# Kernel optimization log

Measured on AMD Instinct MI355X. Metric: run time of the kernel, lower is better.

Reference implementation:

```python
import jax, jax.numpy as jnp
import numpy as np
import math

B_, L_, CSEQ, CMETH = 1, 16384, 5, 3
DM, NL, DI, N, R, K = 256, 6, 512, 16, 32, 4


def setup_inputs():
    key = jax.random.key(0)
    ks = jax.random.split(key, 16)
    s = lambda k, shape, sc=0.02: jax.random.normal(k, shape, jnp.float32) * sc
    # torch-style dt bias init: softplus(bias) in [0.001, 0.1]
    dt_init = jnp.exp(jax.random.uniform(ks[0], (NL, DI)) * (math.log(0.1) - math.log(0.001)) + math.log(0.001))
    dtproj_b = dt_init + jnp.log(-jnp.expm1(-dt_init))
    A = jnp.broadcast_to(jnp.arange(1, N + 1, dtype=jnp.float32), (NL, DI, N))
    return {
        "x": jax.random.uniform(ks[1], (B_, CSEQ, L_), jnp.float32),
        "meth": jax.random.uniform(ks[2], (B_, CMETH, L_), jnp.float32),
        "inp_w": s(ks[3], (CSEQ + CMETH, DM), 0.1),
        "inp_b": jnp.zeros((DM,), jnp.float32),
        "norm_g": jnp.ones((NL, DM), jnp.float32),
        "norm_b": jnp.zeros((NL, DM), jnp.float32),
        "in_proj_w": s(ks[4], (NL, DM, 2 * DI)),
        "conv_w": s(ks[5], (NL, DI, 1, K), 0.1),
        "conv_b": jnp.zeros((NL, DI), jnp.float32),
        "xproj_w": s(ks[6], (NL, DI, R + 2 * N)),
        "dtproj_w": s(ks[7], (NL, R, DI), R ** -0.5),
        "dtproj_b": dtproj_b,
        "A_log": jnp.log(A),
        "Dp": jnp.ones((NL, DI), jnp.float32),
        "outproj_w": s(ks[8], (NL, DI, DM)),
        "fn_g": jnp.ones((DM,), jnp.float32),
        "fn_b": jnp.zeros((DM,), jnp.float32),
        "head_w1": s(ks[9], (DM, DM // 2), DM ** -0.5),
        "head_b1": jnp.zeros((DM // 2,), jnp.float32),
        "head_w2": s(ks[10], (DM // 2, 1), 0.05),
        "head_b2": jnp.zeros((1,), jnp.float32),
    }


def _layernorm(x, g, b, eps=1e-5):
    mu = x.mean(-1, keepdims=True)
    var = ((x - mu) ** 2).mean(-1, keepdims=True)
    return (x - mu) * jax.lax.rsqrt(var + eps) * g + b


def _selective_scan(u, xproj_w, dtproj_w, dtproj_b, A_log, Dp):
    # u: (B, L, DI) -- S6 selective scan (Mamba)
    xdbl = u @ xproj_w                                      # (B,L,R+2N)
    dt_low, Bsel, Csel = jnp.split(xdbl, [R, R + N], axis=-1)
    dt = jax.nn.softplus(dt_low @ dtproj_w + dtproj_b)      # (B,L,DI)
    A = -jnp.exp(A_log)                                     # (DI,N)
    xs = (jnp.swapaxes(dt, 0, 1), jnp.swapaxes(Bsel, 0, 1),
          jnp.swapaxes(Csel, 0, 1), jnp.swapaxes(u, 0, 1))  # each (L,B,...)
    h0 = jnp.zeros((u.shape[0], DI, N), u.dtype)

    def step(h, inp):
        dt_i, B_i, C_i, u_i = inp                           # (B,DI),(B,N),(B,N),(B,DI)
        h = jnp.exp(dt_i[..., None] * A) * h + (dt_i * u_i)[..., None] * B_i[:, None, :]
        y = jnp.einsum('bdn,bn->bd', h, C_i) + Dp * u_i
        return h, y

    _, ys = jax.lax.scan(step, h0, xs)                      # ys: (L,B,DI)
    return jnp.swapaxes(ys, 0, 1)


def _block(x, g, b, wi, cw, cb, xw, dw, db, alog, dp, wo):
    res = x
    x = _layernorm(x, g, b)
    xz = x @ wi                                             # (B,L,2*DI)
    xb, z = jnp.split(xz, 2, axis=-1)
    xb = jnp.swapaxes(xb, 1, 2)                             # (B,DI,L)
    # causal depthwise conv: left-pad K-1 == torch pad both + truncate to L
    xb = jax.lax.conv_general_dilated(xb, cw, (1,), [(K - 1, 0)],
                                      dimension_numbers=('NCH', 'OIH', 'NCH'),
                                      feature_group_count=DI) + cb[:, None]
    xb = jax.nn.silu(jnp.swapaxes(xb, 1, 2))
    y = _selective_scan(xb, xw, dw, db, alog, dp)
    out = (y * jax.nn.silu(z)) @ wo
    return out + res


def reference(x, meth, inp_w, inp_b, norm_g, norm_b, in_proj_w, conv_w, conv_b,
              xproj_w, dtproj_w, dtproj_b, A_log, Dp, outproj_w,
              fn_g, fn_b, head_w1, head_b1, head_w2, head_b2):
    h = jnp.swapaxes(jnp.concatenate([x, meth], axis=1), 1, 2) @ inp_w + inp_b
    for i in range(NL):
        h = _block(h, norm_g[i], norm_b[i], in_proj_w[i], conv_w[i], conv_b[i],
                   xproj_w[i], dtproj_w[i], dtproj_b[i], A_log[i], Dp[i], outproj_w[i])
    h = _layernorm(h, fn_g, fn_b)
    embed = h.mean(axis=1)                                  # pool='mean'
    hid = jax.nn.gelu(embed @ head_w1 + head_b1, approximate=False)
    logits = hid @ head_w2 + head_b2                        # (B,1)
    return logits
```

## Files before the change

### kernel.cpp

```cpp
#include <hip/hip_runtime.h>
#include <math.h>

#define L_SEQ  16384
#define DMODEL 256
#define NLAYER 6
#define DIN    512
#define NSTATE 16
#define RRANK  32
#define CH     16
#define NCH    1024
#define NGRP   32
#define GSZ    32
#define NLOG2E 1.44269504088896340736f

using f16x8 = __attribute__((ext_vector_type(8))) _Float16;
using f32x4 = __attribute__((ext_vector_type(4))) float;

static __device__ __forceinline__ float siluf(float x)
{
    return x / (1.0f + exp2f(x * -NLOG2E));
}

static __device__ __forceinline__ float softplusf(float v)
{
    float t = exp2f(v * NLOG2E);
    float sp = __log2f(1.0f + t) * (1.0f / NLOG2E);
    return (v > 20.0f) ? v : sp;
}

static __device__ __forceinline__ float pow_np1(float a1, int np1)
{
    float a2 = a1 * a1, a4 = a2 * a2, a8 = a4 * a4;
    float a = 1.f;
    if (np1 & 1)  a *= a1;
    if (np1 & 2)  a *= a2;
    if (np1 & 4)  a *= a4;
    if (np1 & 8)  a *= a8;
    if (np1 & 16) a *= a8 * a8;
    return a;
}

static __device__ __forceinline__ void pow_tree(float e1, float* a)
{
    float e2 = e1 * e1, e4 = e2 * e2, e8 = e4 * e4;
    a[0] = e1;       a[1] = e2;       a[2] = e2 * e1;  a[3] = e4;
    a[4] = e4 * e1;  a[5] = e4 * e2;  a[6] = e4 * a[2]; a[7] = e8;
    a[8] = e8 * e1;  a[9] = e8 * e2;  a[10] = e8 * a[2]; a[11] = e8 * e4;
    a[12] = e8 * a[4]; a[13] = e8 * a[5]; a[14] = e8 * a[6]; a[15] = e8 * e8;
}

__global__ void k_input_proj(const float* __restrict__ x, const float* __restrict__ meth,
                             const float* __restrict__ w, const float* __restrict__ b,
                             float* __restrict__ h)
{
    int idx = blockIdx.x * 256 + threadIdx.x;
    int t = idx >> 8, m = idx & 255;
    float acc = b[m];
#pragma unroll
    for (int c = 0; c < 5; ++c) acc = fmaf(x[c * L_SEQ + t], w[c * DMODEL + m], acc);
#pragma unroll
    for (int c = 0; c < 3; ++c) acc = fmaf(meth[c * L_SEQ + t], w[(5 + c) * DMODEL + m], acc);
    h[idx] = acc;
}

__global__ void k_transpose_h(const float* __restrict__ in, _Float16* __restrict__ out,
                              int K, int N)
{
    __shared__ float tile[64][65];
    const float* inp = in + (size_t)blockIdx.z * K * N;
    _Float16* outp  = out + (size_t)blockIdx.z * K * N;
    int tx = threadIdx.x & 63, ty4 = threadIdx.x >> 6;
    int kbase = blockIdx.y * 64, nbase = blockIdx.x * 64;
#pragma unroll
    for (int i = 0; i < 16; ++i) {
        int krow = ty4 + i * 4;
        tile[krow][tx] = inp[(size_t)(kbase + krow) * N + nbase + tx];
    }
    __syncthreads();
#pragma unroll
    for (int i = 0; i < 16; ++i) {
        int nrow = ty4 + i * 4;
        outp[(size_t)(nbase + nrow) * K + kbase + tx] = (_Float16)tile[tx][nrow];
    }
}

__global__ void k_transpose_dw(const float* __restrict__ in, _Float16* __restrict__ out)
{
    int l = blockIdx.x;
    const float* ip = in + (size_t)l * RRANK * DIN;
    _Float16* op = out + (size_t)l * DIN * RRANK;
    for (int base = 0; base < RRANK * DIN; base += 256) {
        int idx = base + threadIdx.x;
        int r = idx >> 9, d = idx & 511;
        op[d * RRANK + r] = (_Float16)ip[idx];
    }
}

__global__ void k_layernorm_h(const float* __restrict__ src, _Float16* __restrict__ dst,
                              const float* __restrict__ g, const float* __restrict__ b)
{
    int t = blockIdx.x, tid = threadIdx.x;
    float v = src[(size_t)t * DMODEL + tid];
    __shared__ float s[8];
    int lane = tid & 63, wid = tid >> 6;
    float xs = v;
#pragma unroll
    for (int off = 32; off; off >>= 1) xs += __shfl_down(xs, off);
    if (lane == 0) s[wid] = xs;
    __syncthreads();
    float mu = (s[0] + s[1] + s[2] + s[3]) * (1.0f / DMODEL);
    float d = v - mu;
    float x2 = d * d;
#pragma unroll
    for (int off = 32; off; off >>= 1) x2 += __shfl_down(x2, off);
    if (lane == 0) s[4 + wid] = x2;
    __syncthreads();
    float var = (s[4] + s[5] + s[6] + s[7]) * (1.0f / DMODEL);
    dst[(size_t)t * DMODEL + tid] = (_Float16)(d * rsqrtf(var + 1e-5f) * g[tid] + b[tid]);
}

__global__ void k_layernorm(const float* __restrict__ src, float* __restrict__ dst,
                            const float* __restrict__ g, const float* __restrict__ b)
{
    int t = blockIdx.x, tid = threadIdx.x;
    float v = src[(size_t)t * DMODEL + tid];
    __shared__ float s[8];
    int lane = tid & 63, wid = tid >> 6;
    float xs = v;
#pragma unroll
    for (int off = 32; off; off >>= 1) xs += __shfl_down(xs, off);
    if (lane == 0) s[wid] = xs;
    __syncthreads();
    float mu = (s[0] + s[1] + s[2] + s[3]) * (1.0f / DMODEL);
    float d = v - mu;
    float x2 = d * d;
#pragma unroll
    for (int off = 32; off; off >>= 1) x2 += __shfl_down(x2, off);
    if (lane == 0) s[4 + wid] = x2;
    __syncthreads();
    float var = (s[4] + s[5] + s[6] + s[7]) * (1.0f / DMODEL);
    dst[(size_t)t * DMODEL + tid] = d * rsqrtf(var + 1e-5f) * g[tid] + b[tid];
}

__launch_bounds__(256)
__global__ void k_gemm1_h(const _Float16* __restrict__ A,
                          const _Float16* __restrict__ B,
                          _Float16* __restrict__ xb,
                          _Float16* __restrict__ z)
{
    const int K = DMODEL;
    __shared__ __align__(16) _Float16 As[128 * 40];
    __shared__ __align__(16) _Float16 Bs[128 * 40];
    int tid = threadIdx.x;
    int row0 = blockIdx.y * 128, col0 = blockIdx.x * 128;
    int lane = tid & 63, wave = tid >> 6;
    int wr = wave >> 1, wc = wave & 1;
    int r = lane & 15, quad = lane >> 4;
    int srow = tid >> 2, sseg = (tid & 3) * 8;
    f32x4 acc[4][4] = {};
    for (int k0 = 0; k0 < K; k0 += 32) {
        __syncthreads();
        f16x8 a0 = *(const f16x8*)(A + (size_t)(row0 + srow) * K + k0 + sseg);
        f16x8 a1 = *(const f16x8*)(A + (size_t)(row0 + srow + 64) * K + k0 + sseg);
        f16x8 b0 = *(const f16x8*)(B + (size_t)(col0 + srow) * K + k0 + sseg);
        f16x8 b1 = *(const f16x8*)(B + (size_t)(col0 + srow + 64) * K + k0 + sseg);
        *(f16x8*)&As[srow * 40 + sseg]        = a0;
        *(f16x8*)&As[(srow + 64) * 40 + sseg] = a1;
        *(f16x8*)&Bs[srow * 40 + sseg]        = b0;
        *(f16x8*)&Bs[(srow + 64) * 40 + sseg] = b1;
        __syncthreads();
        f16x8 af[4], bf[4];
#pragma unroll
        for (int i = 0; i < 4; ++i) af[i] = *(const f16x8*)&As[(wr * 64 + i * 16 + r) * 40 + quad * 8];
#pragma unroll
        for (int j = 0; j < 4; ++j) bf[j] = *(const f16x8*)&Bs[(wc * 64 + j * 16 + r) * 40 + quad * 8];
#pragma unroll
        for (int i = 0; i < 4; ++i)
#pragma unroll
            for (int j = 0; j < 4; ++j)
                acc[i][j] = __builtin_amdgcn_mfma_f32_16x16x32_f16(af[i], bf[j], acc[i][j], 0, 0, 0);
    }
    bool isz = (col0 >= 512);
    _Float16* dst = isz ? z : xb;
    int cbase = isz ? (col0 - 512) : col0;
#pragma unroll
    for (int i = 0; i < 4; ++i)
#pragma unroll
        for (int j = 0; j < 4; ++j) {
            int col = cbase + wc * 64 + j * 16 + r;
#pragma unroll
            for (int g = 0; g < 4; ++g) {
                int row = row0 + wr * 64 + i * 16 + quad * 4 + g;
                dst[(size_t)row * 512 + col] = (_Float16)acc[i][j][g];
            }
        }
}

__launch_bounds__(256)
__global__ void k_gemm_out_h(const _Float16* __restrict__ Y,
                             const _Float16* __restrict__ Z,
                             const _Float16* __restrict__ B,
                             float* __restrict__ H)
{
    const int N = DMODEL, K = DIN;
    __shared__ __align__(16) _Float16 As[128 * 40];
    __shared__ __align__(16) _Float16 Bs[128 * 40];
    int tid = threadIdx.x;
    int row0 = blockIdx.y * 128, col0 = blockIdx.x * 128;
    int lane = tid & 63, wave = tid >> 6;
    int wr = wave >> 1, wc = wave & 1;
    int r = lane & 15, quad = lane >> 4;
    int srow = tid >> 2, sseg = (tid & 3) * 8;
    f32x4 acc[4][4] = {};
    for (int k0 = 0; k0 < K; k0 += 32) {
        __syncthreads();
        f16x8 y0 = *(const f16x8*)(Y + (size_t)(row0 + srow) * DIN + k0 + sseg);
        f16x8 z0 = *(const f16x8*)(Z + (size_t)(row0 + srow) * DIN + k0 + sseg);
        f16x8 y1 = *(const f16x8*)(Y + (size_t)(row0 + srow + 64) * DIN + k0 + sseg);
        f16x8 z1 = *(const f16x8*)(Z + (size_t)(row0 + srow + 64) * DIN + k0 + sseg);
        f16x8 b0 = *(const f16x8*)(B + (size_t)(col0 + srow) * K + k0 + sseg);
        f16x8 b1 = *(const f16x8*)(B + (size_t)(col0 + srow + 64) * K + k0 + sseg);
        f16x8 p0, p1;
#pragma unroll
        for (int e = 0; e < 8; ++e) {
            float zv0 = (float)z0[e], zv1 = (float)z1[e];
            p0[e] = (_Float16)((float)y0[e] * siluf(zv0));
            p1[e] = (_Float16)((float)y1[e] * siluf(zv1));
        }
        *(f16x8*)&As[srow * 40 + sseg]        = p0;
        *(f16x8*)&As[(srow + 64) * 40 + sseg] = p1;
        *(f16x8*)&Bs[srow * 40 + sseg]        = b0;
        *(f16x8*)&Bs[(srow + 64) * 40 + sseg] = b1;
        __syncthreads();
        f16x8 af[4], bf[4];
#pragma unroll
        for (int i = 0; i < 4; ++i) af[i] = *(const f16x8*)&As[(wr * 64 + i * 16 + r) * 40 + quad * 8];
#pragma unroll
        for (int j = 0; j < 4; ++j) bf[j] = *(const f16x8*)&Bs[(wc * 64 + j * 16 + r) * 40 + quad * 8];
#pragma unroll
        for (int i = 0; i < 4; ++i)
#pragma unroll
            for (int j = 0; j < 4; ++j)
                acc[i][j] = __builtin_amdgcn_mfma_f32_16x16x32_f16(af[i], bf[j], acc[i][j], 0, 0, 0);
    }
#pragma unroll
    for (int i = 0; i < 4; ++i)
#pragma unroll
        for (int j = 0; j < 4; ++j) {
            int col = col0 + wc * 64 + j * 16 + r;
#pragma unroll
            for (int g = 0; g < 4; ++g) {
                int row = row0 + wr * 64 + i * 16 + quad * 4 + g;
                H[(size_t)row * N + col] += acc[i][j][g];
            }
        }
}

__launch_bounds__(256)
__global__ void k_xproj_conv(const _Float16* __restrict__ xb, const _Float16* __restrict__ Bw,
                             const float* __restrict__ cw, const float* __restrict__ cb,
                             _Float16* __restrict__ u, float* __restrict__ C,
                             _Float16* __restrict__ dtl)
{
    __shared__ __align__(16) _Float16 As[64 * 72];
    __shared__ __align__(16) _Float16 Bs[64 * 72];
    __shared__ float cwS[4][512];
    __shared__ float cbS[512];
    int tid = threadIdx.x;
    int row0 = blockIdx.x * 64;
    int lane = tid & 63, wave = tid >> 6;
    int r = lane & 15, quad = lane >> 4;
    int srow = tid >> 2, sseg = (tid & 3) * 16;
    int row = row0 + srow;
    for (int i = tid; i < 2048; i += 256) cwS[i & 3][i >> 2] = cw[i];
    for (int i = tid; i < 512; i += 256) cbS[i] = cb[i];
    f32x4 acc[4] = {};
    for (int k0 = 0; k0 < 512; k0 += 64) {
        __syncthreads();
        f16x8 ures[2];
#pragma unroll
        for (int hseg = 0; hseg < 2; ++hseg) {
            int dbase = k0 + sseg + hseg * 8;
            float a[8];
#pragma unroll
            for (int e = 0; e < 8; ++e) a[e] = cbS[dbase + e];
#pragma unroll
            for (int k = 0; k < 4; ++k) {
                int tt = row + k - 3;
                if (tt >= 0) {
                    f16x8 xv = *(const f16x8*)(xb + (size_t)tt * DIN + dbase);
#pragma unroll
                    for (int e = 0; e < 8; ++e)
                        a[e] = fmaf((float)xv[e], cwS[k][dbase + e], a[e]);
                }
            }
#pragma unroll
            for (int e = 0; e < 8; ++e) ures[hseg][e] = (_Float16)siluf(a[e]);
        }
        *(f16x8*)(u + (size_t)row * DIN + k0 + sseg)     = ures[0];
        *(f16x8*)(u + (size_t)row * DIN + k0 + sseg + 8) = ures[1];
        f16x8 b0 = *(const f16x8*)(Bw + (size_t)srow * 512 + k0 + sseg);
        f16x8 b1 = *(const f16x8*)(Bw + (size_t)srow * 512 + k0 + sseg + 8);
        *(f16x8*)&As[srow * 72 + sseg]     = ures[0];
        *(f16x8*)&As[srow * 72 + sseg + 8] = ures[1];
        *(f16x8*)&Bs[srow * 72 + sseg]     = b0;
        *(f16x8*)&Bs[srow * 72 + sseg + 8] = b1;
        __syncthreads();
#pragma unroll
        for (int s = 0; s < 2; ++s) {
            f16x8 af = *(const f16x8*)&As[(wave * 16 + r) * 72 + s * 32 + quad * 8];
#pragma unroll
            for (int j = 0; j < 4; ++j) {
                f16x8 bf = *(const f16x8*)&Bs[(j * 16 + r) * 72 + s * 32 + quad * 8];
                acc[j] = __builtin_amdgcn_mfma_f32_16x16x32_f16(af, bf, acc[j], 0, 0, 0);
            }
        }
    }
#pragma unroll
    for (int j = 0; j < 4; ++j)
#pragma unroll
        for (int g = 0; g < 4; ++g) {
            int orow = row0 + wave * 16 + quad * 4 + g;
            int col = j * 16 + r;
            C[(size_t)orow * 64 + col] = acc[j][g];
            if (j < 2) dtl[(size_t)orow * 32 + col] = (_Float16)acc[j][g];
        }
}

__launch_bounds__(256)
__global__ void k_dt_h(const _Float16* __restrict__ dtl, const _Float16* __restrict__ dwT,
                       const float* __restrict__ db, _Float16* __restrict__ dth)
{
    __shared__ __align__(16) _Float16 tile[64][136];
    int tid = threadIdx.x;
    int lane = tid & 63, wave = tid >> 6;
    int r = lane & 15, quad = lane >> 4;
    int col0 = blockIdx.x * 128, row0 = blockIdx.y * 64;
    f16x8 af = *(const f16x8*)(dtl + (size_t)(row0 + wave * 16 + r) * 32 + quad * 8);
#pragma unroll
    for (int j = 0; j < 8; ++j) {
        int col = col0 + j * 16 + r;
        f16x8 bf = *(const f16x8*)(dwT + (size_t)col * 32 + quad * 8);
        f32x4 acc = {};
        acc = __builtin_amdgcn_mfma_f32_16x16x32_f16(af, bf, acc, 0, 0, 0);
        float bias = db[col];
#pragma unroll
        for (int g = 0; g < 4; ++g) {
            int row = wave * 16 + quad * 4 + g;
            tile[row][j * 16 + r] = (_Float16)softplusf(acc[g] + bias);
        }
    }
    __syncthreads();
    int orow = tid >> 2, oseg = (tid & 3) * 32;
    _Float16* dst = dth + (size_t)(row0 + orow) * 512 + col0 + oseg;
#pragma unroll
    for (int q = 0; q < 4; ++q)
        *(f16x8*)(dst + q * 8) = *(const f16x8*)&tile[orow][oseg + q * 8];
}

__launch_bounds__(256)
__global__ void k_scan_chunk(const _Float16* __restrict__ dth, const _Float16* __restrict__ u,
                             const float* __restrict__ xdbl,
                             float* __restrict__ hend, float* __restrict__ ap1)
{
    int c = blockIdx.x;
    int d = blockIdx.y * 256 + threadIdx.x;
    float h[16] = {};
    float sw = 0.f;
    int t0 = c * CH;
#pragma unroll 4
    for (int i = 0; i < CH; ++i) {
        int t = t0 + i;
        float w  = (float)dth[(size_t)t * 512 + d];
        float uv = (float)u[(size_t)t * DIN + d];
        const float4* Bp = (const float4*)(xdbl + (size_t)t * 64 + 32);
        float Bv[16];
        *(float4*)&Bv[0]  = Bp[0];
        *(float4*)&Bv[4]  = Bp[1];
        *(float4*)&Bv[8]  = Bp[2];
        *(float4*)&Bv[12] = Bp[3];
        sw += w;
        float e1 = exp2f(w * -NLOG2E);
        float bwu = w * uv;
        float a[16];
        pow_tree(e1, a);
#pragma unroll
        for (int n = 0; n < 16; ++n) h[n] = fmaf(a[n], h[n], bwu * Bv[n]);
    }
    float* hp = hend + (size_t)c * (DIN * 16) + (size_t)d * 16;
    *(float4*)&hp[0]  = make_float4(h[0], h[1], h[2], h[3]);
    *(float4*)&hp[4]  = make_float4(h[4], h[5], h[6], h[7]);
    *(float4*)&hp[8]  = make_float4(h[8], h[9], h[10], h[11]);
    *(float4*)&hp[12] = make_float4(h[12], h[13], h[14], h[15]);
    ap1[c * DIN + d] = exp2f(sw * -NLOG2E);
}

__global__ void k_carry_group(float* __restrict__ hend, const float* __restrict__ ap1,
                              float* __restrict__ gsum, float* __restrict__ Acum1,
                              float* __restrict__ a1g)
{
    int g = blockIdx.y;
    int idx = blockIdx.x * 256 + threadIdx.x;
    int d = idx >> 4, np1 = (idx & 15) + 1;
    bool lead = (idx & 15) == 0;
    float carry = 0.f, A1 = 1.f;
    for (int cg = 0; cg < GSZ; ++cg) {
        int c = g * GSZ + cg;
        float a1 = ap1[c * DIN + d];
        if (lead) Acum1[c * DIN + d] = A1;
        A1 *= a1;
        float a = pow_np1(a1, np1);
        int j = c * (DIN * 16) + idx;
        float he = hend[j];
        hend[j] = carry;
        carry = fmaf(a, carry, he);
    }
    gsum[g * (DIN * 16) + idx] = carry;
    if (lead) a1g[g * DIN + d] = A1;
}

__global__ void k_carry_top(const float* __restrict__ gsum, const float* __restrict__ a1g,
                            float* __restrict__ goff)
{
    int idx = blockIdx.x * 256 + threadIdx.x;
    int d = idx >> 4, np1 = (idx & 15) + 1;
    float off = 0.f;
    for (int g = 0; g < NGRP; ++g) {
        goff[g * (DIN * 16) + idx] = off;
        float a = pow_np1(a1g[g * DIN + d], np1);
        off = fmaf(a, off, gsum[g * (DIN * 16) + idx]);
    }
}

__launch_bounds__(256)
__global__ void k_scan_apply(const _Float16* __restrict__ dth, _Float16* __restrict__ u,
                             const float* __restrict__ xdbl,
                             const float* __restrict__ hend, const float* __restrict__ Acum1,
                             const float* __restrict__ goff, const float* __restrict__ Dp)
{
    int c = blockIdx.x, g = c / GSZ;
    int d = blockIdx.y * 256 + threadIdx.x;
    const float* hp = hend + (size_t)c * (DIN * 16) + (size_t)d * 16;
    const float* op = goff + (size_t)g * (DIN * 16) + (size_t)d * 16;
    float h[16], ofs[16], at[16];
    *(float4*)&h[0]  = *(const float4*)&hp[0];
    *(float4*)&h[4]  = *(const float4*)&hp[4];
    *(float4*)&h[8]  = *(const float4*)&hp[8];
    *(float4*)&h[12] = *(const float4*)&hp[12];
    *(float4*)&ofs[0]  = *(const float4*)&op[0];
    *(float4*)&ofs[4]  = *(const float4*)&op[4];
    *(float4*)&ofs[8]  = *(const float4*)&op[8];
    *(float4*)&ofs[12] = *(const float4*)&op[12];
    pow_tree(Acum1[c * DIN + d], at);
#pragma unroll
    for (int n = 0; n < 16; ++n) h[n] = fmaf(at[n], ofs[n], h[n]);
    float Dpd = Dp[d];
    int t0 = c * CH;
#pragma unroll 4
    for (int i = 0; i < CH; ++i) {
        int t = t0 + i;
        float w  = (float)dth[(size_t)t * 512 + d];
        float uv = (float)u[(size_t)t * DIN + d];
        const float4* Bp = (const float4*)(xdbl + (size_t)t * 64 + 32);
        float Bv[16], Cv[16];
        *(float4*)&Bv[0]  = Bp[0];
        *(float4*)&Bv[4]  = Bp[1];
        *(float4*)&Bv[8]  = Bp[2];
        *(float4*)&Bv[12] = Bp[3];
        *(float4*)&Cv[0]  = Bp[4];
        *(float4*)&Cv[4]  = Bp[5];
        *(float4*)&Cv[8]  = Bp[6];
        *(float4*)&Cv[12] = Bp[7];
        float e1 = exp2f(w * -NLOG2E);
        float bwu = w * uv;
        float a[16];
        pow_tree(e1, a);
        float y = 0.f;
#pragma unroll
        for (int n = 0; n < 16; ++n) {
            h[n] = fmaf(a[n], h[n], bwu * Bv[n]);
            y = fmaf(h[n], Cv[n], y);
        }
        u[(size_t)t * DIN + d] = (_Float16)fmaf(Dpd, uv, y);
    }
}

__global__ void k_pool(const float* __restrict__ src, float* __restrict__ embed)
{
    int m = threadIdx.x;
    int t0 = blockIdx.x * 64;
    float acc = 0.f;
    for (int i = 0; i < 64; ++i) acc += src[(size_t)(t0 + i) * DMODEL + m];
    atomicAdd(&embed[m], acc);
}

__global__ void k_head(const float* __restrict__ embed, const float* __restrict__ w1,
                       const float* __restrict__ b1, const float* __restrict__ w2,
                       const float* __restrict__ b2, float* __restrict__ out)
{
    int j = threadIdx.x;
    const float invL = 1.0f / L_SEQ;
    float acc = b1[j];
    for (int k = 0; k < DMODEL; ++k) acc = fmaf(embed[k] * invL, w1[k * 128 + j], acc);
    float g = 0.5f * acc * (1.0f + erff(acc * 0.70710678118654752f));
    float v = g * w2[j];
#pragma unroll
    for (int off = 32; off; off >>= 1) v += __shfl_down(v, off);
    __shared__ float s[2];
    if ((j & 63) == 0) s[j >> 6] = v;
    __syncthreads();
    if (j == 0) out[0] = s[0] + s[1] + b2[0];
}

extern "C" void kernel_launch(void* const* d_in, const int* in_sizes, int n_in,
                              void* d_out, int out_size, void* d_ws, size_t ws_size,
                              hipStream_t stream)
{
    const float* x      = (const float*)d_in[0];
    const float* meth   = (const float*)d_in[1];
    const float* inp_w  = (const float*)d_in[2];
    const float* inp_b  = (const float*)d_in[3];
    const float* norm_g = (const float*)d_in[4];
    const float* norm_b = (const float*)d_in[5];
    const float* wi     = (const float*)d_in[6];
    const float* cw     = (const float*)d_in[7];
    const float* cb     = (const float*)d_in[8];
    const float* xw     = (const float*)d_in[9];
    const float* dw     = (const float*)d_in[10];
    const float* db     = (const float*)d_in[11];
    const float* alog   = (const float*)d_in[12];
    const float* dp     = (const float*)d_in[13];
    const float* wo     = (const float*)d_in[14];
    const float* fn_g   = (const float*)d_in[15];
    const float* fn_b   = (const float*)d_in[16];
    const float* hw1    = (const float*)d_in[17];
    const float* hb1    = (const float*)d_in[18];
    const float* hw2    = (const float*)d_in[19];
    const float* hb2    = (const float*)d_in[20];
    float* out = (float*)d_out;

    float* ws    = (float*)d_ws;
    float* hbuf  = ws;
    float* xln   = hbuf + (size_t)L_SEQ * DMODEL;
    _Float16* xb_h = (_Float16*)(xln + (size_t)L_SEQ * DMODEL);
    _Float16* z_h  = xb_h + (size_t)L_SEQ * DIN;
    _Float16* u_h  = z_h  + (size_t)L_SEQ * DIN;
    _Float16* dth  = u_h  + (size_t)L_SEQ * DIN;
    float* xdbl  = (float*)(dth + (size_t)L_SEQ * DIN);
    float* hend  = xdbl + (size_t)L_SEQ * 64;
    float* ap1   = hend + (size_t)NCH * DIN * 16;
    float* Acum1 = ap1  + (size_t)NCH * DIN;
    float* gsum  = Acum1 + (size_t)NCH * DIN;
    float* goff  = gsum + (size_t)NGRP * DIN * 16;
    float* a1g   = goff + (size_t)NGRP * DIN * 16;
    float* embed = a1g  + (size_t)NGRP * DIN;

    _Float16* xln_h = (_Float16*)xln;
    _Float16* wih   = xln_h + (size_t)L_SEQ * DMODEL;
    _Float16* woh   = wih + (size_t)NLAYER * 1024 * 256;
    _Float16* xwT   = woh + (size_t)NLAYER * DMODEL * DIN;
    _Float16* dtl   = xwT + (size_t)NLAYER * 64 * DIN;
    _Float16* dwT   = dtl + (size_t)L_SEQ * RRANK;

    dim3 b256(256);
    k_input_proj<<<L_SEQ, b256, 0, stream>>>(x, meth, inp_w, inp_b, hbuf);
    k_transpose_h<<<dim3(16, 4, NLAYER), b256, 0, stream>>>(wi, wih, DMODEL, 1024);
    k_transpose_h<<<dim3(4, 8, NLAYER), b256, 0, stream>>>(wo, woh, DIN, DMODEL);
    k_transpose_h<<<dim3(1, 8, NLAYER), b256, 0, stream>>>(xw, xwT, DIN, 64);
    k_transpose_dw<<<NLAYER, b256, 0, stream>>>(dw, dwT);

    for (int l = 0; l < NLAYER; ++l) {
        k_layernorm_h<<<L_SEQ, b256, 0, stream>>>(hbuf, xln_h, norm_g + l * DMODEL, norm_b + l * DMODEL);
        k_gemm1_h<<<dim3(8, 128), b256, 0, stream>>>(
            xln_h, wih + (size_t)l * 1024 * 256, xb_h, z_h);
        k_xproj_conv<<<L_SEQ / 64, b256, 0, stream>>>(
            xb_h, xwT + (size_t)l * 64 * DIN, cw + l * DIN * 4, cb + l * DIN,
            u_h, xdbl, dtl);
        k_dt_h<<<dim3(4, L_SEQ / 64), b256, 0, stream>>>(
            dtl, dwT + (size_t)l * DIN * RRANK, db + l * DIN, dth);
        k_scan_chunk<<<dim3(NCH, DIN / 256), b256, 0, stream>>>(dth, u_h, xdbl, hend, ap1);
        k_carry_group<<<dim3(32, NGRP), b256, 0, stream>>>(hend, ap1, gsum, Acum1, a1g);
        k_carry_top<<<32, b256, 0, stream>>>(gsum, a1g, goff);
        k_scan_apply<<<dim3(NCH, DIN / 256), b256, 0, stream>>>(
            dth, u_h, xdbl, hend, Acum1, goff, dp + l * DIN);
        k_gemm_out_h<<<dim3(2, 128), b256, 0, stream>>>(
            u_h, z_h, woh + (size_t)l * DMODEL * DIN, hbuf);
    }

    k_layernorm<<<L_SEQ, b256, 0, stream>>>(hbuf, xln, fn_g, fn_b);
    hipMemsetAsync(embed, 0, DMODEL * sizeof(float), stream);
    k_pool<<<L_SEQ / 64, b256, 0, stream>>>(xln, embed);
    k_head<<<1, 128, 0, stream>>>(embed, hw1, hb1, hw2, hb2, out);
}
```

Measured before the change: 1.163 ms.

## Fold scan output into local pass and apply carry correction as cheap fixup

The first chunked-scan pass now does the full zero-init local scan and writes partial outputs directly. It also stores the running product of per-step decay as an fp16 array. The old second pass, which redid the full 16-state recurrence, becomes a fixup pass with no recurrence: each step adds C·(decay^n · h_init) to the stored output. The chunk length is doubled (fewer chunks and groups), which cuts the carry-state traffic. In exchange the change adds a new fp16 buffer write/read and a second read-modify-write of u, and fp16 cumulative decays may underflow or lose precision for long chunks.

```diff
diff --git a/kernel.cpp b/kernel.cpp
--- a/kernel.cpp
+++ b/kernel.cpp
@@ -7,9 +7,9 @@
 #define DIN    512
 #define NSTATE 16
 #define RRANK  32
-#define CH     16
-#define NCH    1024
-#define NGRP   32
+#define CH     32
+#define NCH    512
+#define NGRP   16
 #define GSZ    32
 #define NLOG2E 1.44269504088896340736f
 
@@ -359,101 +359,15 @@
 }
 
 __launch_bounds__(256)
-__global__ void k_scan_chunk(const _Float16* __restrict__ dth, const _Float16* __restrict__ u,
-                             const float* __restrict__ xdbl,
-                             float* __restrict__ hend, float* __restrict__ ap1)
+__global__ void k_scan_local(const _Float16* __restrict__ dth, _Float16* __restrict__ u,
+                             const float* __restrict__ xdbl, const float* __restrict__ Dp,
+                             float* __restrict__ hend, float* __restrict__ ap1,
+                             _Float16* __restrict__ swcumh)
 {
     int c = blockIdx.x;
     int d = blockIdx.y * 256 + threadIdx.x;
     float h[16] = {};
-    float sw = 0.f;
-    int t0 = c * CH;
-#pragma unroll 4
-    for (int i = 0; i < CH; ++i) {
-        int t = t0 + i;
-        float w  = (float)dth[(size_t)t * 512 + d];
-        float uv = (float)u[(size_t)t * DIN + d];
-        const float4* Bp = (const float4*)(xdbl + (size_t)t * 64 + 32);
-        float Bv[16];
-        *(float4*)&Bv[0]  = Bp[0];
-        *(float4*)&Bv[4]  = Bp[1];
-        *(float4*)&Bv[8]  = Bp[2];
-        *(float4*)&Bv[12] = Bp[3];
-        sw += w;
-        float e1 = exp2f(w * -NLOG2E);
-        float bwu = w * uv;
-        float a[16];
-        pow_tree(e1, a);
-#pragma unroll
-        for (int n = 0; n < 16; ++n) h[n] = fmaf(a[n], h[n], bwu * Bv[n]);
-    }
-    float* hp = hend + (size_t)c * (DIN * 16) + (size_t)d * 16;
-    *(float4*)&hp[0]  = make_float4(h[0], h[1], h[2], h[3]);
-    *(float4*)&hp[4]  = make_float4(h[4], h[5], h[6], h[7]);
-    *(float4*)&hp[8]  = make_float4(h[8], h[9], h[10], h[11]);
-    *(float4*)&hp[12] = make_float4(h[12], h[13], h[14], h[15]);
-    ap1[c * DIN + d] = exp2f(sw * -NLOG2E);
-}
-
-__global__ void k_carry_group(float* __restrict__ hend, const float* __restrict__ ap1,
-                              float* __restrict__ gsum, float* __restrict__ Acum1,
-                              float* __restrict__ a1g)
-{
-    int g = blockIdx.y;
-    int idx = blockIdx.x * 256 + threadIdx.x;
-    int d = idx >> 4, np1 = (idx & 15) + 1;
-    bool lead = (idx & 15) == 0;
-    float carry = 0.f, A1 = 1.f;
-    for (int cg = 0; cg < GSZ; ++cg) {
-        int c = g * GSZ + cg;
-        float a1 = ap1[c * DIN + d];
-        if (lead) Acum1[c * DIN + d] = A1;
-        A1 *= a1;
-        float a = pow_np1(a1, np1);
-        int j = c * (DIN * 16) + idx;
-        float he = hend[j];
-        hend[j] = carry;
-        carry = fmaf(a, carry, he);
-    }
-    gsum[g * (DIN * 16) + idx] = carry;
-    if (lead) a1g[g * DIN + d] = A1;
-}
-
-__global__ void k_carry_top(const float* __restrict__ gsum, const float* __restrict__ a1g,
-                            float* __restrict__ goff)
-{
-    int idx = blockIdx.x * 256 + threadIdx.x;
-    int d = idx >> 4, np1 = (idx & 15) + 1;
-    float off = 0.f;
-    for (int g = 0; g < NGRP; ++g) {
-        goff[g * (DIN * 16) + idx] = off;
-        float a = pow_np1(a1g[g * DIN + d], np1);
-        off = fmaf(a, off, gsum[g * (DIN * 16) + idx]);
-    }
-}
-
-__launch_bounds__(256)
-__global__ void k_scan_apply(const _Float16* __restrict__ dth, _Float16* __restrict__ u,
-                             const float* __restrict__ xdbl,
-                             const float* __restrict__ hend, const float* __restrict__ Acum1,
-                             const float* __restrict__ goff, const float* __restrict__ Dp)
-{
-    int c = blockIdx.x, g = c / GSZ;
-    int d = blockIdx.y * 256 + threadIdx.x;
-    const float* hp = hend + (size_t)c * (DIN * 16) + (size_t)d * 16;
-    const float* op = goff + (size_t)g * (DIN * 16) + (size_t)d * 16;
-    float h[16], ofs[16], at[16];
-    *(float4*)&h[0]  = *(const float4*)&hp[0];
-    *(float4*)&h[4]  = *(const float4*)&hp[4];
-    *(float4*)&h[8]  = *(const float4*)&hp[8];
-    *(float4*)&h[12] = *(const float4*)&hp[12];
-    *(float4*)&ofs[0]  = *(const float4*)&op[0];
-    *(float4*)&ofs[4]  = *(const float4*)&op[4];
-    *(float4*)&ofs[8]  = *(const float4*)&op[8];
-    *(float4*)&ofs[12] = *(const float4*)&op[12];
-    pow_tree(Acum1[c * DIN + d], at);
-#pragma unroll
-    for (int n = 0; n < 16; ++n) h[n] = fmaf(at[n], ofs[n], h[n]);
+    float e1cum = 1.f;
     float Dpd = Dp[d];
     int t0 = c * CH;
 #pragma unroll 4
@@ -472,6 +386,7 @@
         *(float4*)&Cv[8]  = Bp[6];
         *(float4*)&Cv[12] = Bp[7];
         float e1 = exp2f(w * -NLOG2E);
+        e1cum *= e1;
         float bwu = w * uv;
         float a[16];
         pow_tree(e1, a);
@@ -482,6 +397,93 @@
             y = fmaf(h[n], Cv[n], y);
         }
         u[(size_t)t * DIN + d] = (_Float16)fmaf(Dpd, uv, y);
+        swcumh[(size_t)t * DIN + d] = (_Float16)e1cum;
+    }
+    float* hp = hend + (size_t)c * (DIN * 16) + (size_t)d * 16;
+    *(float4*)&hp[0]  = make_float4(h[0], h[1], h[2], h[3]);
+    *(float4*)&hp[4]  = make_float4(h[4], h[5], h[6], h[7]);
+    *(float4*)&hp[8]  = make_float4(h[8], h[9], h[10], h[11]);
+    *(float4*)&hp[12] = make_float4(h[12], h[13], h[14], h[15]);
+    ap1[c * DIN + d] = e1cum;
+}
+
+__global__ void k_carry_group(float* __restrict__ hend, const float* __restrict__ ap1,
+                              float* __restrict__ gsum, float* __restrict__ Acum1,
+                              float* __restrict__ a1g)
+{
+    int g = blockIdx.y;
+    int idx = blockIdx.x * 256 + threadIdx.x;
+    int d = idx >> 4, np1 = (idx & 15) + 1;
+    bool lead = (idx & 15) == 0;
+    float carry = 0.f, A1 = 1.f;
+    for (int cg = 0; cg < GSZ; ++cg) {
+        int c = g * GSZ + cg;
+        float a1 = ap1[c * DIN + d];
+        if (lead) Acum1[c * DIN + d] = A1;
+        A1 *= a1;
+        float a = pow_np1(a1, np1);
+        int j = c * (DIN * 16) + idx;
+        float he = hend[j];
+        hend[j] = carry;
+        carry = fmaf(a, carry, he);
+    }
+    gsum[g * (DIN * 16) + idx] = carry;
+    if (lead) a1g[g * DIN + d] = A1;
+}
+
+__global__ void k_carry_top(const float* __restrict__ gsum, const float* __restrict__ a1g,
+                            float* __restrict__ goff)
+{
+    int idx = blockIdx.x * 256 + threadIdx.x;
+    int d = idx >> 4, np1 = (idx & 15) + 1;
+    float off = 0.f;
+#pragma unroll
+    for (int g = 0; g < NGRP; ++g) {
+        goff[g * (DIN * 16) + idx] = off;
+        float a = pow_np1(a1g[g * DIN + d], np1);
+        off = fmaf(a, off, gsum[g * (DIN * 16) + idx]);
+    }
+}
+
+__launch_bounds__(256)
+__global__ void k_scan_fix(_Float16* __restrict__ u, const float* __restrict__ xdbl,
+                           const float* __restrict__ hend, const float* __restrict__ Acum1,
+                           const float* __restrict__ goff, const _Float16* __restrict__ swcumh)
+{
+    int c = blockIdx.x, g = c / GSZ;
+    int d = blockIdx.y * 256 + threadIdx.x;
+    const float* hp = hend + (size_t)c * (DIN * 16) + (size_t)d * 16;
+    const float* op = goff + (size_t)g * (DIN * 16) + (size_t)d * 16;
+    float hinit[16], ofs[16], at[16];
+    *(float4*)&hinit[0]  = *(const float4*)&hp[0];
+    *(float4*)&hinit[4]  = *(const float4*)&hp[4];
+    *(float4*)&hinit[8]  = *(const float4*)&hp[8];
+    *(float4*)&hinit[12] = *(const float4*)&hp[12];
+    *(float4*)&ofs[0]  = *(const float4*)&op[0];
+    *(float4*)&ofs[4]  = *(const float4*)&op[4];
+    *(float4*)&ofs[8]  = *(const float4*)&op[8];
+    *(float4*)&ofs[12] = *(const float4*)&op[12];
+    pow_tree(Acum1[c * DIN + d], at);
+#pragma unroll
+    for (int n = 0; n < 16; ++n) hinit[n] = fmaf(at[n], ofs[n], hinit[n]);
+    int t0 = c * CH;
+#pragma unroll 4
+    for (int i = 0; i < CH; ++i) {
+        int t = t0 + i;
+        float e1c = (float)swcumh[(size_t)t * DIN + d];
+        const float4* Bp = (const float4*)(xdbl + (size_t)t * 64 + 48);
+        float Cv[16];
+        *(float4*)&Cv[0]  = Bp[0];
+        *(float4*)&Cv[4]  = Bp[1];
+        *(float4*)&Cv[8]  = Bp[2];
+        *(float4*)&Cv[12] = Bp[3];
+        float pw[16];
+        pow_tree(e1c, pw);
+        float y = (float)u[(size_t)t * DIN + d];
+#pragma unroll
+        for (int n = 0; n < 16; ++n)
+            y = fmaf(pw[n] * hinit[n], Cv[n], y);
+        u[(size_t)t * DIN + d] = (_Float16)y;
     }
 }
 
@@ -546,7 +548,8 @@
     _Float16* z_h  = xb_h + (size_t)L_SEQ * DIN;
     _Float16* u_h  = z_h  + (size_t)L_SEQ * DIN;
     _Float16* dth  = u_h  + (size_t)L_SEQ * DIN;
-    float* xdbl  = (float*)(dth + (size_t)L_SEQ * DIN);
+    _Float16* swcumh = dth + (size_t)L_SEQ * DIN;
+    float* xdbl  = (float*)(swcumh + (size_t)L_SEQ * DIN);
     float* hend  = xdbl + (size_t)L_SEQ * 64;
     float* ap1   = hend + (size_t)NCH * DIN * 16;
     float* Acum1 = ap1  + (size_t)NCH * DIN;
@@ -578,11 +581,12 @@
             u_h, xdbl, dtl);
         k_dt_h<<<dim3(4, L_SEQ / 64), b256, 0, stream>>>(
             dtl, dwT + (size_t)l * DIN * RRANK, db + l * DIN, dth);
-        k_scan_chunk<<<dim3(NCH, DIN / 256), b256, 0, stream>>>(dth, u_h, xdbl, hend, ap1);
+        k_scan_local<<<dim3(NCH, DIN / 256), b256, 0, stream>>>(
+            dth, u_h, xdbl, dp + l * DIN, hend, ap1, swcumh);
         k_carry_group<<<dim3(32, NGRP), b256, 0, stream>>>(hend, ap1, gsum, Acum1, a1g);
         k_carry_top<<<32, b256, 0, stream>>>(gsum, a1g, goff);
-        k_scan_apply<<<dim3(NCH, DIN / 256), b256, 0, stream>>>(
-            dth, u_h, xdbl, hend, Acum1, goff, dp + l * DIN);
+        k_scan_fix<<<dim3(NCH, DIN / 256), b256, 0, stream>>>(
+            u_h, xdbl, hend, Acum1, goff, swcumh);
         k_gemm_out_h<<<dim3(2, 128), b256, 0, stream>>>(
             u_h, z_h, woh + (size_t)l * DMODEL * DIN, hbuf);
     }
```

Result: faster. 1.137 ms (-2.3%).
